# Performance work log

Measured on AMD Instinct MI355X. Metric: run time of the kernel, lower is better.

The kernel has to match this reference:

```python
import jax, jax.numpy as jnp
import numpy as np

B, S, D, H = 2, 2048, 512, 8
DK = D // H


def setup_inputs() -> dict:
    key = jax.random.key(0)
    ks = jax.random.split(key, 7)
    scale = 1.0 / np.sqrt(D)
    return {
        "query": jax.random.normal(ks[0], (B, S, D), dtype=jnp.float32),
        "key": jax.random.normal(ks[1], (B, S, D), dtype=jnp.float32),
        "value": jax.random.normal(ks[2], (B, S, D), dtype=jnp.float32),
        "w_q": jax.random.normal(ks[3], (D, D), dtype=jnp.float32) * scale,
        "w_k": jax.random.normal(ks[4], (D, D), dtype=jnp.float32) * scale,
        "w_v": jax.random.normal(ks[5], (D, D), dtype=jnp.float32) * scale,
        "w_o": jax.random.normal(ks[6], (D, D), dtype=jnp.float32) * scale,
    }


def reference(query, key, value, w_q, w_k, w_v, w_o):
    # Linear projections (torch nn.Linear: x @ W.T), split into heads -> [b, h, s, dk]
    def proj(x, w):
        return (x @ w.T).reshape(B, -1, H, DK).transpose(0, 2, 1, 3)

    q = proj(query, w_q)
    k = proj(key, w_k)
    v = proj(value, w_v)

    # scaled dot-product attention (unfused, materializes [b,h,s,s] scores)
    scores = jnp.einsum("bhqd,bhkd->bhqk", q, k) / np.sqrt(DK)
    p_attn = jax.nn.softmax(scores, axis=-1)
    out = jnp.einsum("bhqk,bhkd->bhqd", p_attn, v)  # [b,h,s,dk]

    # merge heads and final projection
    out = out.transpose(0, 2, 1, 3).reshape(B, -1, D)
    out = out @ w_o.T
    return (out, p_attn)
```

## Files before the change

### kernel.cpp

```cpp
#include <hip/hip_runtime.h>
#include <hip/hip_bf16.h>
#include <cstdint>
#include <cstddef>

#define BB 2
#define SS 2048
#define DD 512
#define HH 8
#define DKK 64

typedef __attribute__((ext_vector_type(8))) short bf16x8;
typedef __attribute__((ext_vector_type(4))) float f32x4;

__device__ __forceinline__ unsigned short f2bf(float f) {
    union { float f; unsigned u; } v; v.f = f;
    unsigned u = v.u;
    return (unsigned short)((u + 0x7fffu + ((u >> 16) & 1u)) >> 16);
}
__device__ __forceinline__ unsigned pack2(float a, float b) {
    return (unsigned)f2bf(a) | ((unsigned)f2bf(b) << 16);
}

typedef const __attribute__((address_space(1))) unsigned int* gp_t;
typedef __attribute__((address_space(3))) unsigned int* lp_t;
__device__ __forceinline__ void gload_lds16(const void* g, void* l) {
    __builtin_amdgcn_global_load_lds((gp_t)g, (lp_t)l, 16, 0, 0);
}

__global__ __launch_bounds__(256) void k_cvt(
    const float* __restrict__ q, const float* __restrict__ k, const float* __restrict__ v,
    const float* __restrict__ wq, const float* __restrict__ wk, const float* __restrict__ wv,
    const float* __restrict__ wo, unsigned short* __restrict__ dst)
{
    const size_t NX = (size_t)BB * SS * DD;
    const size_t NW = (size_t)DD * DD;
    const int y = blockIdx.y;
    const float* src; unsigned short* d; int n;
    switch (y) {
        case 0: src = q;  d = dst;                 n = (int)NX; break;
        case 1: src = k;  d = dst + NX;            n = (int)NX; break;
        case 2: src = v;  d = dst + 2 * NX;        n = (int)NX; break;
        case 3: src = wq; d = dst + 3 * NX;        n = (int)NW; break;
        case 4: src = wk; d = dst + 3 * NX + NW;   n = (int)NW; break;
        case 5: src = wv; d = dst + 3 * NX + 2*NW; n = (int)NW; break;
        default: src = wo; d = dst + 3 * NX + 3*NW; n = (int)NW; break;
    }
    int idx = (blockIdx.x * 256 + threadIdx.x) * 8;
    if (idx >= n) return;
    float4 a = *(const float4*)(src + idx);
    float4 b = *(const float4*)(src + idx + 4);
    *(uint4*)(d + idx) = make_uint4(pack2(a.x,a.y), pack2(a.z,a.w), pack2(b.x,b.y), pack2(b.z,b.w));
}

template <int MODE>
__global__ __launch_bounds__(256) void k_gemm64(
    const unsigned short* __restrict__ A, const unsigned short* __restrict__ W,
    unsigned short* __restrict__ dbf, float* __restrict__ df)
{
    __shared__ unsigned short smem[8192];
    const int bm = blockIdx.x, bn = blockIdx.y;
    const int tid = threadIdx.x, w = tid >> 6, lane = tid & 63, quad = lane >> 4, l15 = lane & 15;

    f32x4 acc[4];
    #pragma unroll
    for (int i = 0; i < 4; ++i) acc[i] = (f32x4){0.f, 0.f, 0.f, 0.f};

    for (int k0 = 0; k0 < DD; k0 += 64) {
        #pragma unroll
        for (int r = 0; r < 2; ++r) {
            int flat = r * 256 + tid;
            int row = flat >> 3, c = flat & 7, cs = c ^ (row & 7);
            gload_lds16(A + (size_t)(bm * 64 + row) * DD + k0 + cs * 8, &smem[flat * 8]);
        }
        #pragma unroll
        for (int r = 0; r < 2; ++r) {
            int flat = r * 256 + tid;
            int row = flat >> 3, c = flat & 7, cs = c ^ (row & 7);
            gload_lds16(W + (size_t)(bn * 64 + row) * DD + k0 + cs * 8, &smem[4096 + flat * 8]);
        }
        __syncthreads();
        int mrow = w * 16 + l15;
        bf16x8 a0 = *(const bf16x8*)&smem[(mrow * 8 + (quad ^ (mrow & 7))) * 8];
        bf16x8 a1 = *(const bf16x8*)&smem[(mrow * 8 + ((quad + 4) ^ (mrow & 7))) * 8];
        #pragma unroll
        for (int nt = 0; nt < 4; ++nt) {
            int nrow = nt * 16 + l15;
            bf16x8 b0 = *(const bf16x8*)&smem[4096 + (nrow * 8 + (quad ^ (nrow & 7))) * 8];
            bf16x8 b1 = *(const bf16x8*)&smem[4096 + (nrow * 8 + ((quad + 4) ^ (nrow & 7))) * 8];
            acc[nt] = __builtin_amdgcn_mfma_f32_16x16x32_bf16(a0, b0, acc[nt], 0, 0, 0);
            acc[nt] = __builtin_amdgcn_mfma_f32_16x16x32_bf16(a1, b1, acc[nt], 0, 0, 0);
        }
        __syncthreads();
    }

    if (MODE == 0 || MODE == 1) {
        const float sc = (MODE == 0) ? 0.125f : 1.0f;
        #pragma unroll
        for (int nt = 0; nt < 4; ++nt) {
            int n = bn * 64 + nt * 16 + l15;
            int h = n >> 6, dk = n & 63;
            #pragma unroll
            for (int rg = 0; rg < 4; ++rg) {
                int m = bm * 64 + w * 16 + quad * 4 + rg;
                int b = m >> 11, s = m & (SS - 1);
                dbf[(((size_t)(b * HH + h) * SS + s) << 6) + dk] = f2bf(acc[nt][rg] * sc);
            }
        }
    } else if (MODE == 2) {
        unsigned short* T = smem;
        #pragma unroll
        for (int nt = 0; nt < 4; ++nt)
            #pragma unroll
            for (int rg = 0; rg < 4; ++rg)
                T[(w * 16 + quad * 4 + rg) * 72 + nt * 16 + l15] = f2bf(acc[nt][rg]);
        __syncthreads();
        int n = tid >> 2, s0 = (tid & 3) * 16;
        int ng = bn * 64 + n, h = ng >> 6, dk = ng & 63;
        int mg = bm * 64 + s0, b = mg >> 11, s = mg & (SS - 1);
        unsigned vals[8];
        #pragma unroll
        for (int i = 0; i < 8; ++i)
            vals[i] = (unsigned)T[(s0 + 2*i) * 72 + n] | ((unsigned)T[(s0 + 2*i + 1) * 72 + n] << 16);
        unsigned short* dp = dbf + ((size_t)(b * HH + h) * DKK + dk) * SS + s;
        ((uint4*)dp)[0] = make_uint4(vals[0], vals[1], vals[2], vals[3]);
        ((uint4*)dp)[1] = make_uint4(vals[4], vals[5], vals[6], vals[7]);
    } else {
        #pragma unroll
        for (int nt = 0; nt < 4; ++nt)
            #pragma unroll
            for (int rg = 0; rg < 4; ++rg)
                df[(size_t)(bm * 64 + w * 16 + quad * 4 + rg) * DD + bn * 64 + nt * 16 + l15] =
                    acc[nt][rg];
    }
}

__global__ __launch_bounds__(256) void k_attn(
    const unsigned short* __restrict__ Qw, const unsigned short* __restrict__ Kw,
    const unsigned short* __restrict__ Vt, unsigned short* __restrict__ AO,
    float* __restrict__ Linv)
{
    __shared__ unsigned short Pl[2][4][16][68];
    const int qt = blockIdx.x, bh = blockIdx.y;
    const int tid = threadIdx.x, w = tid >> 6, lane = tid & 63, quad = lane >> 4, l15 = lane & 15;

    const unsigned short* Qb = Qw + ((size_t)bh * SS + qt * 64 + w * 16) * DKK;
    const unsigned short* Kb = Kw + (size_t)bh * SS * DKK;
    const unsigned short* Vb = Vt + (size_t)bh * DKK * SS;

    bf16x8 qa0 = *(const bf16x8*)&Qb[l15 * DKK + quad * 8];
    bf16x8 qa1 = *(const bf16x8*)&Qb[l15 * DKK + 32 + quad * 8];

    f32x4 oacc[4];
    #pragma unroll
    for (int i = 0; i < 4; ++i) oacc[i] = (f32x4){0.f, 0.f, 0.f, 0.f};
    float lsum[4] = {0.f, 0.f, 0.f, 0.f};

    #pragma unroll 2
    for (int kt = 0; kt < SS / 64; ++kt) {
        const int buf = kt & 1;
        const unsigned short* Kt = Kb + (size_t)kt * 64 * DKK;
        f32x4 sa[4];
        #pragma unroll
        for (int i = 0; i < 4; ++i) sa[i] = (f32x4){0.f, 0.f, 0.f, 0.f};
        #pragma unroll
        for (int jt = 0; jt < 4; ++jt) {
            bf16x8 b0 = *(const bf16x8*)&Kt[(jt * 16 + l15) * DKK + quad * 8];
            bf16x8 b1 = *(const bf16x8*)&Kt[(jt * 16 + l15) * DKK + 32 + quad * 8];
            sa[jt] = __builtin_amdgcn_mfma_f32_16x16x32_bf16(qa0, b0, sa[jt], 0, 0, 0);
            sa[jt] = __builtin_amdgcn_mfma_f32_16x16x32_bf16(qa1, b1, sa[jt], 0, 0, 0);
        }
        float ev[4][4];
        #pragma unroll
        for (int jt = 0; jt < 4; ++jt)
            #pragma unroll
            for (int rg = 0; rg < 4; ++rg)
                ev[jt][rg] = __expf(sa[jt][rg]);
        #pragma unroll
        for (int rg = 0; rg < 4; ++rg) {
            float s = ev[0][rg] + ev[1][rg] + ev[2][rg] + ev[3][rg];
            s += __shfl_xor(s, 1);
            s += __shfl_xor(s, 2);
            s += __shfl_xor(s, 4);
            s += __shfl_xor(s, 8);
            lsum[rg] += s;
        }
        #pragma unroll
        for (int jt = 0; jt < 4; ++jt)
            #pragma unroll
            for (int rg = 0; rg < 4; ++rg)
                Pl[buf][w][quad * 4 + rg][jt * 16 + l15] = f2bf(ev[jt][rg]);
        bf16x8 pa0 = *(const bf16x8*)&Pl[buf][w][l15][quad * 8];
        bf16x8 pa1 = *(const bf16x8*)&Pl[buf][w][l15][32 + quad * 8];
        #pragma unroll
        for (int dt = 0; dt < 4; ++dt) {
            const unsigned short* Vp = Vb + (size_t)(dt * 16 + l15) * SS + kt * 64;
            bf16x8 v0 = *(const bf16x8*)&Vp[quad * 8];
            bf16x8 v1 = *(const bf16x8*)&Vp[32 + quad * 8];
            oacc[dt] = __builtin_amdgcn_mfma_f32_16x16x32_bf16(pa0, v0, oacc[dt], 0, 0, 0);
            oacc[dt] = __builtin_amdgcn_mfma_f32_16x16x32_bf16(pa1, v1, oacc[dt], 0, 0, 0);
        }
    }

    float linv[4];
    #pragma unroll
    for (int rg = 0; rg < 4; ++rg) linv[rg] = 1.0f / lsum[rg];

    const int b = bh >> 3, h = bh & 7;
    const int srow = qt * 64 + w * 16 + quad * 4;
    #pragma unroll
    for (int dt = 0; dt < 4; ++dt)
        #pragma unroll
        for (int rg = 0; rg < 4; ++rg)
            AO[((size_t)(b * SS + srow + rg) << 9) + h * 64 + dt * 16 + l15] =
                f2bf(oacc[dt][rg] * linv[rg]);

    if (l15 == 0) {
        #pragma unroll
        for (int rg = 0; rg < 4; ++rg)
            Linv[(size_t)bh * SS + srow + rg] = linv[rg];
    }
}

__global__ __launch_bounds__(256) void k_pwrite(
    const unsigned short* __restrict__ Qw, const unsigned short* __restrict__ Kw,
    const float* __restrict__ Linv, float* __restrict__ P)
{
    const int qt = blockIdx.x, bh = blockIdx.y, ks = blockIdx.z;
    const int tid = threadIdx.x, w = tid >> 6, lane = tid & 63, quad = lane >> 4, l15 = lane & 15;

    const unsigned short* Qb = Qw + ((size_t)bh * SS + qt * 64 + w * 16) * DKK;
    bf16x8 qa0 = *(const bf16x8*)&Qb[l15 * DKK + quad * 8];
    bf16x8 qa1 = *(const bf16x8*)&Qb[l15 * DKK + 32 + quad * 8];

    float linv[4];
    #pragma unroll
    for (int rg = 0; rg < 4; ++rg)
        linv[rg] = Linv[(size_t)bh * SS + qt * 64 + w * 16 + quad * 4 + rg];

    const unsigned short* Kb = Kw + (size_t)bh * SS * DKK + (size_t)ks * 512 * DKK;
    float* Pb = P + (((size_t)bh * SS + qt * 64 + w * 16 + quad * 4) << 11) + ks * 512;

    for (int kt = 0; kt < 8; ++kt) {
        const unsigned short* Kt = Kb + (size_t)kt * 64 * DKK;
        #pragma unroll
        for (int jt = 0; jt < 4; ++jt) {
            bf16x8 b0 = *(const bf16x8*)&Kt[(jt * 16 + l15) * DKK + quad * 8];
            bf16x8 b1 = *(const bf16x8*)&Kt[(jt * 16 + l15) * DKK + 32 + quad * 8];
            f32x4 sa = (f32x4){0.f, 0.f, 0.f, 0.f};
            sa = __builtin_amdgcn_mfma_f32_16x16x32_bf16(qa0, b0, sa, 0, 0, 0);
            sa = __builtin_amdgcn_mfma_f32_16x16x32_bf16(qa1, b1, sa, 0, 0, 0);
            #pragma unroll
            for (int rg = 0; rg < 4; ++rg)
                Pb[((size_t)rg << 11) + kt * 64 + jt * 16 + l15] = __expf(sa[rg]) * linv[rg];
        }
    }
}

extern "C" void kernel_launch(void* const* d_in, const int* in_sizes, int n_in,
                              void* d_out, int out_size, void* d_ws, size_t ws_size,
                              hipStream_t stream) {
    const float* q  = (const float*)d_in[0];
    const float* k  = (const float*)d_in[1];
    const float* v  = (const float*)d_in[2];
    const float* wq = (const float*)d_in[3];
    const float* wk = (const float*)d_in[4];
    const float* wv = (const float*)d_in[5];
    const float* wo = (const float*)d_in[6];

    float* out = (float*)d_out;
    float* P   = out + (size_t)BB * SS * DD;

    const size_t NX = (size_t)BB * SS * DD;
    const size_t NW = (size_t)DD * DD;
    unsigned short* scratch = (unsigned short*)P;
    unsigned short* Xq = scratch;
    unsigned short* Xk = scratch + NX;
    unsigned short* Xv = scratch + 2 * NX;
    unsigned short* Wq = scratch + 3 * NX;
    unsigned short* Wk = Wq + NW;
    unsigned short* Wv = Wk + NW;
    unsigned short* Wo = Wv + NW;
    unsigned short* AO = Wo + NW;

    unsigned short* Qw = (unsigned short*)d_ws;
    unsigned short* Kw = Qw + NX;
    unsigned short* Vt = Kw + NX;
    float* Linv = (float*)(Vt + NX);

    k_cvt<<<dim3(1024, 7), 256, 0, stream>>>(q, k, v, wq, wk, wv, wo, scratch);
    k_gemm64<0><<<dim3(64, 8), 256, 0, stream>>>(Xq, Wq, Qw, nullptr);
    k_gemm64<1><<<dim3(64, 8), 256, 0, stream>>>(Xk, Wk, Kw, nullptr);
    k_gemm64<2><<<dim3(64, 8), 256, 0, stream>>>(Xv, Wv, Vt, nullptr);
    k_attn<<<dim3(SS / 64, BB * HH), 256, 0, stream>>>(Qw, Kw, Vt, AO, Linv);
    k_gemm64<3><<<dim3(64, 8), 256, 0, stream>>>(AO, Wo, nullptr, out);
    k_pwrite<<<dim3(SS / 64, BB * HH, 4), 256, 0, stream>>>(Qw, Kw, Linv, P);
}
```

Baseline: 487.2 us.

## Fuse P-matrix write into attention kernel and batch QKV projections

Merges the three QKV projection GEMMs into one launch using blockIdx.z. The probability-matrix write kernel is folded into the tail of the attention kernel, which recomputes QK^T and writes normalized exp scores with nontemporal stores. AO and Wo now live in workspace, since P is overwritten inside the attention kernel. This removes launches and the Linv round trip, at the cost of a longer attention kernel that runs with fewer blocks (512 vs 2048 for the P write), which may reduce parallelism for the store-bound P output.

New measurement: 460.4 us. -5.5%, faster.

```diff
diff --git a/kernel.cpp b/kernel.cpp
--- a/kernel.cpp
+++ b/kernel.cpp
@@ -30,7 +30,8 @@
 __global__ __launch_bounds__(256) void k_cvt(
     const float* __restrict__ q, const float* __restrict__ k, const float* __restrict__ v,
     const float* __restrict__ wq, const float* __restrict__ wk, const float* __restrict__ wv,
-    const float* __restrict__ wo, unsigned short* __restrict__ dst)
+    const float* __restrict__ wo, unsigned short* __restrict__ dst,
+    unsigned short* __restrict__ dwo)
 {
     const size_t NX = (size_t)BB * SS * DD;
     const size_t NW = (size_t)DD * DD;
@@ -43,7 +44,7 @@
         case 3: src = wq; d = dst + 3 * NX;        n = (int)NW; break;
         case 4: src = wk; d = dst + 3 * NX + NW;   n = (int)NW; break;
         case 5: src = wv; d = dst + 3 * NX + 2*NW; n = (int)NW; break;
-        default: src = wo; d = dst + 3 * NX + 3*NW; n = (int)NW; break;
+        default: src = wo; d = dwo;                n = (int)NW; break;
     }
     int idx = (blockIdx.x * 256 + threadIdx.x) * 8;
     if (idx >= n) return;
@@ -52,19 +53,11 @@
     *(uint4*)(d + idx) = make_uint4(pack2(a.x,a.y), pack2(a.z,a.w), pack2(b.x,b.y), pack2(b.z,b.w));
 }
 
-template <int MODE>
-__global__ __launch_bounds__(256) void k_gemm64(
+__device__ __forceinline__ void gemm64_core(
     const unsigned short* __restrict__ A, const unsigned short* __restrict__ W,
-    unsigned short* __restrict__ dbf, float* __restrict__ df)
-{
-    __shared__ unsigned short smem[8192];
-    const int bm = blockIdx.x, bn = blockIdx.y;
-    const int tid = threadIdx.x, w = tid >> 6, lane = tid & 63, quad = lane >> 4, l15 = lane & 15;
-
-    f32x4 acc[4];
-    #pragma unroll
-    for (int i = 0; i < 4; ++i) acc[i] = (f32x4){0.f, 0.f, 0.f, 0.f};
-
+    unsigned short* smem, int bm, int bn, int tid, f32x4 acc[4])
+{
+    const int w = tid >> 6, lane = tid & 63, quad = lane >> 4, l15 = lane & 15;
     for (int k0 = 0; k0 < DD; k0 += 64) {
         #pragma unroll
         for (int r = 0; r < 2; ++r) {
@@ -92,9 +85,29 @@
         }
         __syncthreads();
     }
-
-    if (MODE == 0 || MODE == 1) {
-        const float sc = (MODE == 0) ? 0.125f : 1.0f;
+}
+
+__global__ __launch_bounds__(256) void k_gemm_qkv(
+    const unsigned short* __restrict__ scratch,
+    unsigned short* __restrict__ Qw, unsigned short* __restrict__ Kw,
+    unsigned short* __restrict__ Vt)
+{
+    __shared__ unsigned short smem[8192];
+    const size_t NX = (size_t)BB * SS * DD, NW = (size_t)DD * DD;
+    const int z = blockIdx.z;
+    const unsigned short* A = scratch + (size_t)z * NX;
+    const unsigned short* W = scratch + 3 * NX + (size_t)z * NW;
+    const int bm = blockIdx.x, bn = blockIdx.y;
+    const int tid = threadIdx.x, w = tid >> 6, lane = tid & 63, quad = lane >> 4, l15 = lane & 15;
+
+    f32x4 acc[4];
+    #pragma unroll
+    for (int i = 0; i < 4; ++i) acc[i] = (f32x4){0.f, 0.f, 0.f, 0.f};
+    gemm64_core(A, W, smem, bm, bn, tid, acc);
+
+    if (z != 2) {
+        const float sc = (z == 0) ? 0.125f : 1.0f;
+        unsigned short* dbf = (z == 0) ? Qw : Kw;
         #pragma unroll
         for (int nt = 0; nt < 4; ++nt) {
             int n = bn * 64 + nt * 16 + l15;
@@ -106,7 +119,7 @@
                 dbf[(((size_t)(b * HH + h) * SS + s) << 6) + dk] = f2bf(acc[nt][rg] * sc);
             }
         }
-    } else if (MODE == 2) {
+    } else {
         unsigned short* T = smem;
         #pragma unroll
         for (int nt = 0; nt < 4; ++nt)
@@ -121,23 +134,16 @@
         #pragma unroll
         for (int i = 0; i < 8; ++i)
             vals[i] = (unsigned)T[(s0 + 2*i) * 72 + n] | ((unsigned)T[(s0 + 2*i + 1) * 72 + n] << 16);
-        unsigned short* dp = dbf + ((size_t)(b * HH + h) * DKK + dk) * SS + s;
+        unsigned short* dp = Vt + ((size_t)(b * HH + h) * DKK + dk) * SS + s;
         ((uint4*)dp)[0] = make_uint4(vals[0], vals[1], vals[2], vals[3]);
         ((uint4*)dp)[1] = make_uint4(vals[4], vals[5], vals[6], vals[7]);
-    } else {
-        #pragma unroll
-        for (int nt = 0; nt < 4; ++nt)
-            #pragma unroll
-            for (int rg = 0; rg < 4; ++rg)
-                df[(size_t)(bm * 64 + w * 16 + quad * 4 + rg) * DD + bn * 64 + nt * 16 + l15] =
-                    acc[nt][rg];
-    }
-}
-
-__global__ __launch_bounds__(256) void k_attn(
+    }
+}
+
+__global__ __launch_bounds__(256) void k_attn2(
     const unsigned short* __restrict__ Qw, const unsigned short* __restrict__ Kw,
     const unsigned short* __restrict__ Vt, unsigned short* __restrict__ AO,
-    float* __restrict__ Linv)
+    float* __restrict__ P)
 {
     __shared__ unsigned short Pl[2][4][16][68];
     const int qt = blockIdx.x, bh = blockIdx.y;
@@ -214,33 +220,9 @@
             AO[((size_t)(b * SS + srow + rg) << 9) + h * 64 + dt * 16 + l15] =
                 f2bf(oacc[dt][rg] * linv[rg]);
 
-    if (l15 == 0) {
-        #pragma unroll
-        for (int rg = 0; rg < 4; ++rg)
-            Linv[(size_t)bh * SS + srow + rg] = linv[rg];
-    }
-}
-
-__global__ __launch_bounds__(256) void k_pwrite(
-    const unsigned short* __restrict__ Qw, const unsigned short* __restrict__ Kw,
-    const float* __restrict__ Linv, float* __restrict__ P)
-{
-    const int qt = blockIdx.x, bh = blockIdx.y, ks = blockIdx.z;
-    const int tid = threadIdx.x, w = tid >> 6, lane = tid & 63, quad = lane >> 4, l15 = lane & 15;
-
-    const unsigned short* Qb = Qw + ((size_t)bh * SS + qt * 64 + w * 16) * DKK;
-    bf16x8 qa0 = *(const bf16x8*)&Qb[l15 * DKK + quad * 8];
-    bf16x8 qa1 = *(const bf16x8*)&Qb[l15 * DKK + 32 + quad * 8];
-
-    float linv[4];
-    #pragma unroll
-    for (int rg = 0; rg < 4; ++rg)
-        linv[rg] = Linv[(size_t)bh * SS + qt * 64 + w * 16 + quad * 4 + rg];
-
-    const unsigned short* Kb = Kw + (size_t)bh * SS * DKK + (size_t)ks * 512 * DKK;
-    float* Pb = P + (((size_t)bh * SS + qt * 64 + w * 16 + quad * 4) << 11) + ks * 512;
-
-    for (int kt = 0; kt < 8; ++kt) {
+    float* Pb = P + (((size_t)bh * SS + srow) << 11);
+    #pragma unroll 2
+    for (int kt = 0; kt < SS / 64; ++kt) {
         const unsigned short* Kt = Kb + (size_t)kt * 64 * DKK;
         #pragma unroll
         for (int jt = 0; jt < 4; ++jt) {
@@ -251,9 +233,29 @@
             sa = __builtin_amdgcn_mfma_f32_16x16x32_bf16(qa1, b1, sa, 0, 0, 0);
             #pragma unroll
             for (int rg = 0; rg < 4; ++rg)
-                Pb[((size_t)rg << 11) + kt * 64 + jt * 16 + l15] = __expf(sa[rg]) * linv[rg];
-        }
-    }
+                __builtin_nontemporal_store(__expf(sa[rg]) * linv[rg],
+                    &Pb[((size_t)rg << 11) + kt * 64 + jt * 16 + l15]);
+        }
+    }
+}
+
+__global__ __launch_bounds__(256) void k_gemm_o(
+    const unsigned short* __restrict__ A, const unsigned short* __restrict__ W,
+    float* __restrict__ out)
+{
+    __shared__ unsigned short smem[8192];
+    const int bm = blockIdx.x, bn = blockIdx.y;
+    const int tid = threadIdx.x, w = tid >> 6, lane = tid & 63, quad = lane >> 4, l15 = lane & 15;
+    f32x4 acc[4];
+    #pragma unroll
+    for (int i = 0; i < 4; ++i) acc[i] = (f32x4){0.f, 0.f, 0.f, 0.f};
+    gemm64_core(A, W, smem, bm, bn, tid, acc);
+    #pragma unroll
+    for (int nt = 0; nt < 4; ++nt)
+        #pragma unroll
+        for (int rg = 0; rg < 4; ++rg)
+            out[(size_t)(bm * 64 + w * 16 + quad * 4 + rg) * DD + bn * 64 + nt * 16 + l15] =
+                acc[nt][rg];
 }
 
 extern "C" void kernel_launch(void* const* d_in, const int* in_sizes, int n_in,
@@ -272,26 +274,17 @@
 
     const size_t NX = (size_t)BB * SS * DD;
     const size_t NW = (size_t)DD * DD;
+
     unsigned short* scratch = (unsigned short*)P;
-    unsigned short* Xq = scratch;
-    unsigned short* Xk = scratch + NX;
-    unsigned short* Xv = scratch + 2 * NX;
-    unsigned short* Wq = scratch + 3 * NX;
-    unsigned short* Wk = Wq + NW;
-    unsigned short* Wv = Wk + NW;
-    unsigned short* Wo = Wv + NW;
-    unsigned short* AO = Wo + NW;
-
-    unsigned short* Qw = (unsigned short*)d_ws;
-    unsigned short* Kw = Qw + NX;
-    unsigned short* Vt = Kw + NX;
-    float* Linv = (float*)(Vt + NX);
-
-    k_cvt<<<dim3(1024, 7), 256, 0, stream>>>(q, k, v, wq, wk, wv, wo, scratch);
-    k_gemm64<0><<<dim3(64, 8), 256, 0, stream>>>(Xq, Wq, Qw, nullptr);
-    k_gemm64<1><<<dim3(64, 8), 256, 0, stream>>>(Xk, Wk, Kw, nullptr);
-    k_gemm64<2><<<dim3(64, 8), 256, 0, stream>>>(Xv, Wv, Vt, nullptr);
-    k_attn<<<dim3(SS / 64, BB * HH), 256, 0, stream>>>(Qw, Kw, Vt, AO, Linv);
-    k_gemm64<3><<<dim3(64, 8), 256, 0, stream>>>(AO, Wo, nullptr, out);
-    k_pwrite<<<dim3(SS / 64, BB * HH, 4), 256, 0, stream>>>(Qw, Kw, Linv, P);
-}
+
+    unsigned short* Qw  = (unsigned short*)d_ws;
+    unsigned short* Kw  = Qw + NX;
+    unsigned short* Vt  = Kw + NX;
+    unsigned short* AO  = Vt + NX;
+    unsigned short* Wo2 = AO + NX;
+
+    k_cvt<<<dim3(1024, 7), 256, 0, stream>>>(q, k, v, wq, wk, wv, wo, scratch, Wo2);
+    k_gemm_qkv<<<dim3(64, 8, 3), 256, 0, stream>>>(scratch, Qw, Kw, Vt);
+    k_attn2<<<dim3(SS / 64, BB * HH), 256, 0, stream>>>(Qw, Kw, Vt, AO, P);
+    k_gemm_o<<<dim3(64, 8), 256, 0, stream>>>(AO, Wo2, out);
+}
```
